# Optimization experiments

Measured on AMD Instinct MI355X. Metric: run time of the kernel, lower is better.

Reference implementation:

```python
import jax, jax.numpy as jnp
import numpy as np

B, T, D = 2, 2048, 1024
H, HD = 16, 64
DL, DC = 512, 256
THETA = 10000.0
LN_EPS = 1e-5


def setup_inputs() -> dict:
    key = jax.random.key(0)
    ks = jax.random.split(key, 8)
    s = 0.02
    return {
        "x": jax.random.normal(ks[0], (B, T, D), jnp.float32),
        "W_q": jax.random.normal(ks[1], (H * HD, D), jnp.float32) * s,
        "b_q": jnp.zeros((H * HD,), jnp.float32),
        "W_kvl": jax.random.normal(ks[2], (DL, D), jnp.float32) * s,
        "b_kvl": jnp.zeros((DL,), jnp.float32),
        "ts_scale": jnp.ones((DL,), jnp.float32),
        "ts_shift": jnp.zeros((DL,), jnp.float32),
        "W_comp": jax.random.normal(ks[3], (DC, DL), jnp.float32) * s,
        "W_exp": jax.random.normal(ks[4], (DL, DC), jnp.float32) * s,
        "ln_g": jnp.ones((DC,), jnp.float32),
        "ln_b": jnp.zeros((DC,), jnp.float32),
        "W_fkv": jax.random.normal(ks[5], (2 * H * HD, DL), jnp.float32) * s,
        "b_fkv": jnp.zeros((2 * H * HD,), jnp.float32),
        "W_out": jax.random.normal(ks[6], (D, H * HD), jnp.float32) * s,
        "b_out": jnp.zeros((D,), jnp.float32),
    }


def _rope_tables(t_len):
    inv_freq = 1.0 / (THETA ** (jnp.arange(0, HD, 2, dtype=jnp.float32) / HD))
    pos = jnp.arange(t_len, dtype=jnp.float32)
    freqs = pos[:, None] * inv_freq[None, :]          # [T, HD/2]
    cos = jnp.concatenate([jnp.cos(freqs)] * 2, -1)   # [T, HD]
    sin = jnp.concatenate([jnp.sin(freqs)] * 2, -1)
    return cos[None, None], sin[None, None]           # [1,1,T,HD]


def _rotate_half(z):
    return jnp.concatenate([-z[..., HD // 2:], z[..., :HD // 2]], -1)


def reference(x, W_q, b_q, W_kvl, b_kvl, ts_scale, ts_shift, W_comp, W_exp,
              ln_g, ln_b, W_fkv, b_fkv, W_out, b_out):
    # Q path: [B,T,D] -> [B,H,T,HD]
    q = (jnp.einsum('btd,ed->bte', x, W_q) + b_q).reshape(B, T, H, HD).transpose(0, 2, 1, 3)

    # KV latent + learned KVSplice bottleneck
    kvl = jnp.einsum('btd,ld->btl', x, W_kvl) + b_kvl                 # [B,T,DL]
    xt = kvl * jax.nn.softplus(ts_scale) + ts_shift
    c = jnp.einsum('btl,cl->btc', xt, W_comp)                         # [B,T,DC]
    mu = jnp.mean(c, -1, keepdims=True)
    var = jnp.mean(jnp.square(c - mu), -1, keepdims=True)
    c = (c - mu) * jax.lax.rsqrt(var + LN_EPS) * ln_g + ln_b
    dec = jnp.einsum('btc,lc->btl', c, W_exp)                         # [B,T,DL]

    # Decompress latent to K,V
    kv = jnp.einsum('btl,el->bte', dec, W_fkv) + b_fkv                # [B,T,2*H*HD]
    kv = kv.reshape(B, T, 2, H, HD).transpose(2, 0, 3, 1, 4)          # [2,B,H,T,HD]
    k, v = kv[0], kv[1]

    # RoPE
    cos, sin = _rope_tables(T)
    q = q * cos + _rotate_half(q) * sin
    k = k * cos + _rotate_half(k) * sin

    # Causal SDPA
    scale = 1.0 / np.sqrt(HD)
    scores = jnp.einsum('bhqd,bhkd->bhqk', q, k) * scale
    mask = jnp.tril(jnp.ones((T, T), bool))
    scores = jnp.where(mask, scores, jnp.float32(-1e30))
    attn = jax.nn.softmax(scores, axis=-1)
    o = jnp.einsum('bhqk,bhkd->bhqd', attn, v)
    o = o.transpose(0, 2, 1, 3).reshape(B, T, H * HD)
    return jnp.einsum('bte,de->btd', o, W_out) + b_out
```

## Files before the change

### kernel.cpp

```cpp
#include <hip/hip_runtime.h>
#include <math.h>

#define B_SZ   2
#define T_SEQ  2048
#define NH     16
#define HDIM   64
#define D_MOD  1024
#define DL     512
#define DC     256
#define MROWS  4096

typedef __attribute__((ext_vector_type(8))) short bf16x8;
typedef __attribute__((ext_vector_type(4))) float f32x4;

#define SCALE_Q 0.18033688011112042f

static __device__ __forceinline__ unsigned short f2bf(float f) {
    union { float f; unsigned u; } v; v.f = f;
    unsigned r = v.u + 0x7fffu + ((v.u >> 16) & 1u);
    return (unsigned short)(r >> 16);
}

static __device__ __forceinline__ void gl_lds16(const unsigned short* g,
                                                unsigned short* l) {
    __builtin_amdgcn_global_load_lds(
        (const __attribute__((address_space(1))) unsigned int*)g,
        (__attribute__((address_space(3))) unsigned int*)l, 16, 0, 0);
}

__global__ __launch_bounds__(256) void cvt_bf16(
    const float* __restrict__ x,  const float* __restrict__ wq,
    const float* __restrict__ wkvl, const float* __restrict__ wcomp,
    const float* __restrict__ wexp, const float* __restrict__ wfkv,
    const float* __restrict__ wout,
    unsigned short* __restrict__ xb,  unsigned short* __restrict__ wqh,
    unsigned short* __restrict__ wkvlh, unsigned short* __restrict__ wcomph,
    unsigned short* __restrict__ wexph, unsigned short* __restrict__ wfkvh,
    unsigned short* __restrict__ wouth, float2* __restrict__ rope_tab)
{
    const int g = blockIdx.x * 256 + threadIdx.x;
    const int stride = gridDim.x * 256;
#define CVT_SEG(src, dst, n4)                                              \
    for (int i = g; i < (n4); i += stride) {                               \
        float4 v = ((const float4*)(src))[i];                              \
        unsigned short h[4] = {f2bf(v.x), f2bf(v.y), f2bf(v.z), f2bf(v.w)};\
        *(uint2*)((dst) + (size_t)i * 4) = *(uint2*)h;                     \
    }
    CVT_SEG(x, xb, 1048576)
    CVT_SEG(wq, wqh, 262144)
    CVT_SEG(wkvl, wkvlh, 131072)
    CVT_SEG(wcomp, wcomph, 32768)
    CVT_SEG(wexp, wexph, 32768)
    CVT_SEG(wfkv, wfkvh, 262144)
    CVT_SEG(wout, wouth, 262144)
#undef CVT_SEG
    for (int i = g; i < T_SEQ * 32; i += stride) {
        const int t = i >> 5, fi = i & 31;
        const float inv = __expf((float)fi * (-9.210340371976184f / 32.0f));
        float sn, cs; sincosf((float)t * inv, &sn, &cs);
        rope_tab[i] = make_float2(cs, sn);
    }
}

#define GEMM64P_PROLOG(Aptr, Wptr, Kdim)                                       \
    __shared__ unsigned short As[2][64 * 64];                                  \
    __shared__ unsigned short Ws[2][64 * 64];                                  \
    const int tid = threadIdx.x;                                               \
    const int w = tid >> 6, lane = tid & 63;                                   \
    const int l16 = lane & 15, quad = lane >> 4;                               \
    const int sw8 = ((lane & 7) ^ ((lane >> 3) & 7)) << 3;                     \
    const int srow = lane >> 3;                                                \
    const unsigned short* Ag0 = (Aptr) + (size_t)(m0 + w * 16 + srow) * (Kdim) + sw8;      \
    const unsigned short* Ag1 = Ag0 + (size_t)8 * (Kdim);                      \
    const unsigned short* Wg0 = (Wptr) + (size_t)(n0 + w * 16 + srow) * (Kdim) + sw8;      \
    const unsigned short* Wg1 = Wg0 + (size_t)8 * (Kdim);                      \
    const int aoff = (w * 16) * 64;                                            \
    const int xh = (l16 & 7);                                                  \
    f32x4 acc[4];                                                              \
    _Pragma("unroll") for (int j = 0; j < 4; ++j)                              \
        acc[j] = (f32x4){0.f, 0.f, 0.f, 0.f};                                  \
    gl_lds16(Ag0, &As[0][aoff]);                                               \
    gl_lds16(Ag1, &As[0][aoff + 512]);                                         \
    gl_lds16(Wg0, &Ws[0][aoff]);                                               \
    gl_lds16(Wg1, &Ws[0][aoff + 512]);                                         \
    for (int k0 = 0, buf = 0; k0 < (Kdim); k0 += 64, buf ^= 1) {               \
        if (k0 + 64 < (Kdim)) {                                                \
            gl_lds16(Ag0 + k0 + 64, &As[buf ^ 1][aoff]);                       \
            gl_lds16(Ag1 + k0 + 64, &As[buf ^ 1][aoff + 512]);                 \
            gl_lds16(Wg0 + k0 + 64, &Ws[buf ^ 1][aoff]);                       \
            gl_lds16(Wg1 + k0 + 64, &Ws[buf ^ 1][aoff + 512]);                 \
            asm volatile("s_waitcnt vmcnt(4)" ::: "memory");                   \
        } else {                                                               \
            asm volatile("s_waitcnt vmcnt(0)" ::: "memory");                   \
        }                                                                      \
        __builtin_amdgcn_s_barrier();                                          \
        bf16x8 af[2], bfr[4][2];                                               \
        _Pragma("unroll") for (int kk = 0; kk < 2; ++kk)                       \
            af[kk] = *(const bf16x8*)&As[buf][(w * 16 + l16) * 64 +            \
                                         (((kk * 4 + quad) ^ xh) << 3)];       \
        _Pragma("unroll") for (int j = 0; j < 4; ++j)                          \
            _Pragma("unroll") for (int kk = 0; kk < 2; ++kk)                   \
                bfr[j][kk] = *(const bf16x8*)&Ws[buf][(j * 16 + l16) * 64 +    \
                                             (((kk * 4 + quad) ^ xh) << 3)];   \
        _Pragma("unroll") for (int kk = 0; kk < 2; ++kk)                       \
            _Pragma("unroll") for (int j = 0; j < 4; ++j)                      \
                acc[j] = __builtin_amdgcn_mfma_f32_16x16x32_bf16(              \
                    af[kk], bfr[j][kk], acc[j], 0, 0, 0);                      \
        asm volatile("s_waitcnt lgkmcnt(0)" ::: "memory");                     \
        __builtin_amdgcn_s_barrier();                                          \
    }

#define GEMM128x64P_PROLOG(Aptr, Wptr, Kdim)                                   \
    __shared__ unsigned short As[2][128 * 64];                                 \
    __shared__ unsigned short Ws[2][64 * 64];                                  \
    const int tid = threadIdx.x;                                               \
    const int w = tid >> 6, lane = tid & 63;                                   \
    const int l16 = lane & 15, quad = lane >> 4;                               \
    const int srow = lane >> 3;                                                \
    const int sw8 = ((lane & 7) ^ srow) << 3;                                  \
    const unsigned short* Ag = (Aptr) + (size_t)(m0 + w * 32 + srow) * (Kdim) + sw8; \
    const unsigned short* Wg = (Wptr) + (size_t)(n0 + w * 16 + srow) * (Kdim) + sw8; \
    const int xh = (l16 & 7);                                                  \
    f32x4 acc[2][4];                                                           \
    _Pragma("unroll") for (int mi = 0; mi < 2; ++mi)                           \
        _Pragma("unroll") for (int j = 0; j < 4; ++j)                          \
            acc[mi][j] = (f32x4){0.f, 0.f, 0.f, 0.f};                          \
    _Pragma("unroll") for (int seg = 0; seg < 4; ++seg)                        \
        gl_lds16(Ag + (size_t)(seg * 8) * (Kdim), &As[0][(w * 32 + seg * 8) * 64]); \
    _Pragma("unroll") for (int seg = 0; seg < 2; ++seg)                        \
        gl_lds16(Wg + (size_t)(seg * 8) * (Kdim), &Ws[0][(w * 16 + seg * 8) * 64]); \
    for (int k0 = 0, buf = 0; k0 < (Kdim); k0 += 64, buf ^= 1) {               \
        if (k0 + 64 < (Kdim)) {                                                \
            _Pragma("unroll") for (int seg = 0; seg < 4; ++seg)                \
                gl_lds16(Ag + (size_t)(seg * 8) * (Kdim) + k0 + 64,            \
                         &As[buf ^ 1][(w * 32 + seg * 8) * 64]);               \
            _Pragma("unroll") for (int seg = 0; seg < 2; ++seg)                \
                gl_lds16(Wg + (size_t)(seg * 8) * (Kdim) + k0 + 64,            \
                         &Ws[buf ^ 1][(w * 16 + seg * 8) * 64]);               \
            asm volatile("s_waitcnt vmcnt(6)" ::: "memory");                   \
        } else {                                                               \
            asm volatile("s_waitcnt vmcnt(0)" ::: "memory");                   \
        }                                                                      \
        __builtin_amdgcn_s_barrier();                                          \
        bf16x8 af[2][2], bfr[4][2];                                            \
        _Pragma("unroll") for (int mi = 0; mi < 2; ++mi)                       \
            _Pragma("unroll") for (int kk = 0; kk < 2; ++kk)                   \
                af[mi][kk] = *(const bf16x8*)&As[buf][(w * 32 + mi * 16 + l16) * 64 + \
                                             (((kk * 4 + quad) ^ xh) << 3)];   \
        _Pragma("unroll") for (int j = 0; j < 4; ++j)                          \
            _Pragma("unroll") for (int kk = 0; kk < 2; ++kk)                   \
                bfr[j][kk] = *(const bf16x8*)&Ws[buf][(j * 16 + l16) * 64 +    \
                                             (((kk * 4 + quad) ^ xh) << 3)];   \
        _Pragma("unroll") for (int kk = 0; kk < 2; ++kk)                       \
            _Pragma("unroll") for (int mi = 0; mi < 2; ++mi)                   \
                _Pragma("unroll") for (int j = 0; j < 4; ++j)                  \
                    acc[mi][j] = __builtin_amdgcn_mfma_f32_16x16x32_bf16(      \
                        af[mi][kk], bfr[j][kk], acc[mi][j], 0, 0, 0);          \
        asm volatile("s_waitcnt lgkmcnt(0)" ::: "memory");                     \
        __builtin_amdgcn_s_barrier();                                          \
    }

__global__ __launch_bounds__(256, 3) void gemm_qxt(
    const unsigned short* __restrict__ A, const unsigned short* __restrict__ Wq,
    const unsigned short* __restrict__ Wkvl,
    const float* __restrict__ b_q, const float* __restrict__ b_kvl,
    const float* __restrict__ ts_scale, const float* __restrict__ ts_shift,
    const float2* __restrict__ tab,
    unsigned short* __restrict__ qh, unsigned short* __restrict__ xt)
{
    const int m0 = blockIdx.x * 128;
    const bool is_q = (blockIdx.y < 16);
    const int n0 = is_q ? blockIdx.y * 64 : (blockIdx.y - 16) * 64;
    const unsigned short* W = is_q ? Wq : Wkvl;

    GEMM128x64P_PROLOG(A, W, D_MOD)

    if (is_q) {
#pragma unroll
        for (int j = 0; j < 4; ++j) {
            const int col = n0 + j * 16 + l16;
            const int h = col >> 6, hd = col & 63;
            const float bv = b_q[col];
            const float bvp = b_q[col ^ 32];
            const float sgn = (hd < 32) ? -1.f : 1.f;
#pragma unroll
            for (int mi = 0; mi < 2; ++mi) {
#pragma unroll
                for (int reg = 0; reg < 4; ++reg) {
                    const int row = m0 + w * 32 + mi * 16 + quad * 4 + reg;
                    const int b = row >> 11, t = row & (T_SEQ - 1);
                    const float2 cssn = tab[t * 32 + (hd & 31)];
                    const float v  = acc[mi][j][reg] + bv;
                    const float vp = acc[mi][j ^ 2][reg] + bvp;
                    const float r = (v * cssn.x + sgn * vp * cssn.y) * SCALE_Q;
                    qh[(((size_t)b * NH + h) * T_SEQ + t) * HDIM + hd] = f2bf(r);
                }
            }
        }
    } else {
#pragma unroll
        for (int j = 0; j < 4; ++j) {
            const int col = n0 + j * 16 + l16;
            const float bv = b_kvl[col];
            const float sp_s = log1pf(expf(ts_scale[col]));
            const float sp_t = ts_shift[col];
#pragma unroll
            for (int mi = 0; mi < 2; ++mi) {
#pragma unroll
                for (int reg = 0; reg < 4; ++reg) {
                    const int row = m0 + w * 32 + mi * 16 + quad * 4 + reg;
                    const float val = (acc[mi][j][reg] + bv) * sp_s + sp_t;
                    xt[(size_t)row * DL + col] = f2bf(val);
                }
            }
        }
    }
}

__global__ __launch_bounds__(256, 3) void gemm_kv(
    const unsigned short* __restrict__ A, const unsigned short* __restrict__ W,
    const float* __restrict__ bias, const float2* __restrict__ tab,
    unsigned short* __restrict__ kh, unsigned short* __restrict__ vth)
{
    const int m0 = blockIdx.x * 128, n0 = blockIdx.y * 64;

    GEMM128x64P_PROLOG(A, W, DL)

    if (n0 < 1024) {
#pragma unroll
        for (int j = 0; j < 4; ++j) {
            const int col = n0 + j * 16 + l16;
            const int h = (col >> 6) & 15, hd = col & 63;
            const float bv = bias[col];
            const float bvp = bias[col ^ 32];
            const float sgn = (hd < 32) ? -1.f : 1.f;
#pragma unroll
            for (int mi = 0; mi < 2; ++mi) {
#pragma unroll
                for (int reg = 0; reg < 4; ++reg) {
                    const int row = m0 + w * 32 + mi * 16 + quad * 4 + reg;
                    const int b = row >> 11, t = row & (T_SEQ - 1);
                    const float2 cssn = tab[t * 32 + (hd & 31)];
                    const float v  = acc[mi][j][reg] + bv;
                    const float vp = acc[mi][j ^ 2][reg] + bvp;
                    const float r = v * cssn.x + sgn * vp * cssn.y;
                    kh[(((size_t)b * NH + h) * T_SEQ + t) * HDIM + hd] = f2bf(r);
                }
            }
        }
    } else {
#pragma unroll
        for (int j = 0; j < 4; ++j) {
            const int col = n0 + j * 16 + l16;
            const int cv = col - 1024;
            const int h = cv >> 6, hd = cv & 63;
            const float bv = bias[col];
#pragma unroll
            for (int mi = 0; mi < 2; ++mi) {
                unsigned short hv[4];
                const int r0 = m0 + w * 32 + mi * 16 + quad * 4;
                const int b = r0 >> 11, t0 = r0 & (T_SEQ - 1);
#pragma unroll
                for (int reg = 0; reg < 4; ++reg)
                    hv[reg] = f2bf(acc[mi][j][reg] + bv);
                *(uint2*)&vth[(((size_t)b * NH + h) * HDIM + hd) * T_SEQ + t0] =
                    *(uint2*)hv;
            }
        }
    }
}

__global__ __launch_bounds__(256, 3) void gemm_out(
    const unsigned short* __restrict__ A, const unsigned short* __restrict__ W,
    const float* __restrict__ bias, float* __restrict__ C)
{
    const int m0 = blockIdx.x * 128, n0 = blockIdx.y * 64;

    GEMM128x64P_PROLOG(A, W, D_MOD)

#pragma unroll
    for (int j = 0; j < 4; ++j) {
        const int col = n0 + j * 16 + l16;
        const float bv = bias[col];
#pragma unroll
        for (int mi = 0; mi < 2; ++mi) {
#pragma unroll
            for (int reg = 0; reg < 4; ++reg) {
                const int row = m0 + w * 32 + mi * 16 + quad * 4 + reg;
                C[(size_t)row * D_MOD + col] = acc[mi][j][reg] + bv;
            }
        }
    }
}

__global__ __launch_bounds__(256) void gemm_b(
    const unsigned short* __restrict__ A, const unsigned short* __restrict__ W,
    unsigned short* __restrict__ dec)
{
    const int m0 = blockIdx.x * 64, n0 = blockIdx.y * 64;

    GEMM64P_PROLOG(A, W, DC)

#pragma unroll
    for (int j = 0; j < 4; ++j) {
        const int col = n0 + j * 16 + l16;
#pragma unroll
        for (int reg = 0; reg < 4; ++reg) {
            const int row = m0 + w * 16 + quad * 4 + reg;
            dec[(size_t)row * DL + col] = f2bf(acc[j][reg]);
        }
    }
}

__global__ __launch_bounds__(256) void gemm_c_ln(
    const unsigned short* __restrict__ A, const unsigned short* __restrict__ W,
    const float* __restrict__ g, const float* __restrict__ bta,
    unsigned short* __restrict__ outb)
{
    __shared__ unsigned short As[2][16 * 32];
    __shared__ unsigned short Ws[2][256 * 32];
    __shared__ float redS[4][16];
    __shared__ float redQ[4][16];

    const int tid = threadIdx.x;
    const int w = tid >> 6, lane = tid & 63;
    const int l16 = lane & 15, quad = lane >> 4;
    const int m0 = blockIdx.x * 16;

    const int srow = lane >> 2, scol = (lane & 3) << 3;
    const unsigned short* Ag = A + (size_t)(m0 + srow) * DL + scol;
    const unsigned short* Wg = W + (size_t)(w * 64 + srow) * DL + scol;

    f32x4 acc[4];
#pragma unroll
    for (int j = 0; j < 4; ++j) acc[j] = (f32x4){0.f, 0.f, 0.f, 0.f};

    if (w == 0) gl_lds16(Ag, &As[0][0]);
#pragma unroll
    for (int c = 0; c < 4; ++c)
        gl_lds16(Wg + (size_t)(c * 16) * DL, &Ws[0][(w * 64 + c * 16) * 32]);

    for (int k0 = 0, buf = 0; k0 < DL; k0 += 32, buf ^= 1) {
        if (k0 + 32 < DL) {
            if (w == 0) gl_lds16(Ag + k0 + 32, &As[buf ^ 1][0]);
#pragma unroll
            for (int c = 0; c < 4; ++c)
                gl_lds16(Wg + (size_t)(c * 16) * DL + k0 + 32,
                         &Ws[buf ^ 1][(w * 64 + c * 16) * 32]);
            if (w == 0) {
                asm volatile("s_waitcnt vmcnt(5)" ::: "memory");
            } else {
                asm volatile("s_waitcnt vmcnt(4)" ::: "memory");
            }
        } else {
            asm volatile("s_waitcnt vmcnt(0)" ::: "memory");
        }
        __builtin_amdgcn_s_barrier();

        const bf16x8 af = *(const bf16x8*)&As[buf][l16 * 32 + quad * 8];
        bf16x8 bfr[4];
#pragma unroll
        for (int j = 0; j < 4; ++j)
            bfr[j] = *(const bf16x8*)&Ws[buf][(w * 64 + j * 16 + l16) * 32 + quad * 8];
#pragma unroll
        for (int j = 0; j < 4; ++j)
            acc[j] = __builtin_amdgcn_mfma_f32_16x16x32_bf16(af, bfr[j], acc[j], 0, 0, 0);

        asm volatile("s_waitcnt lgkmcnt(0)" ::: "memory");
        __builtin_amdgcn_s_barrier();
    }

    float s[4], q2[4];
#pragma unroll
    for (int reg = 0; reg < 4; ++reg) {
        float sv = (acc[0][reg] + acc[1][reg]) + (acc[2][reg] + acc[3][reg]);
        float qv = (acc[0][reg] * acc[0][reg] + acc[1][reg] * acc[1][reg]) +
                   (acc[2][reg] * acc[2][reg] + acc[3][reg] * acc[3][reg]);
#pragma unroll
        for (int off = 1; off < 16; off <<= 1) {
            sv += __shfl_xor(sv, off);
            qv += __shfl_xor(qv, off);
        }
        s[reg] = sv; q2[reg] = qv;
    }
    if (l16 == 0) {
#pragma unroll
        for (int reg = 0; reg < 4; ++reg) {
            redS[w][quad * 4 + reg] = s[reg];
            redQ[w][quad * 4 + reg] = q2[reg];
        }
    }
    __syncthreads();

#pragma unroll
    for (int reg = 0; reg < 4; ++reg) {
        const int r = quad * 4 + reg;
        const float sum = (redS[0][r] + redS[1][r]) + (redS[2][r] + redS[3][r]);
        const float sq  = (redQ[0][r] + redQ[1][r]) + (redQ[2][r] + redQ[3][r]);
        const float mu  = sum * (1.0f / DC);
        const float var = sq * (1.0f / DC) - mu * mu;
        const float rstd = rsqrtf(var + 1e-5f);
#pragma unroll
        for (int j = 0; j < 4; ++j) {
            const int col = w * 64 + j * 16 + l16;
            const float val = (acc[j][reg] - mu) * rstd * g[col] + bta[col];
            outb[(size_t)(m0 + r) * DC + col] = f2bf(val);
        }
    }
}

__global__ __launch_bounds__(256, 4) void flash_mfma(
    const unsigned short* __restrict__ q, const unsigned short* __restrict__ k,
    const unsigned short* __restrict__ vt, unsigned short* __restrict__ o)
{
    __shared__ unsigned short Ks[2][64 * 64];
    __shared__ unsigned short Vs[2][64 * 64];
    __shared__ unsigned short Ps[64 * 64];

    const int bh = blockIdx.x & 31;
    const int j  = 31 - (blockIdx.x >> 5);
    const int q0 = j * 64;
    const int tid = threadIdx.x;
    const int w = tid >> 6, lane = tid & 63;
    const int l16 = lane & 15, quad = lane >> 4;
    const int rbase = q0 + w * 16;
    const int xh = l16 & 7;

    bf16x8 qf[2];
#pragma unroll
    for (int kk = 0; kk < 2; ++kk)
        qf[kk] = *(const bf16x8*)(q + ((size_t)bh * T_SEQ + rbase + l16) * HDIM + kk * 32 + quad * 8);

    f32x4 of[4];
    float lrow[4];
#pragma unroll
    for (int dt = 0; dt < 4; ++dt) of[dt] = (f32x4){0.f, 0.f, 0.f, 0.f};
#pragma unroll
    for (int r = 0; r < 4; ++r) lrow[r] = 0.f;

    const int ldr = tid >> 2;
    const int ldc = (tid & 3) * 16;
    const int sg0 = (((ldc >> 3) + 0) ^ (ldr & 7)) << 3;
    const int sg1 = (((ldc >> 3) + 1) ^ (ldr & 7)) << 3;
    const unsigned short* kgb = k + ((size_t)bh * T_SEQ + ldr) * HDIM + ldc;
    const unsigned short* vgb = vt + ((size_t)bh * HDIM + ldr) * T_SEQ + ldc;

    bf16x8 kr0 = *(const bf16x8*)kgb;
    bf16x8 kr1 = *(const bf16x8*)(kgb + 8);
    bf16x8 vr0 = *(const bf16x8*)vgb;
    bf16x8 vr1 = *(const bf16x8*)(vgb + 8);

    const int kend = (j + 1) * 64;
    int buf = 0;
    for (int k0 = 0; k0 < kend; k0 += 64, buf ^= 1) {
        *(bf16x8*)&Ks[buf][ldr * 64 + sg0] = kr0;
        *(bf16x8*)&Ks[buf][ldr * 64 + sg1] = kr1;
        *(bf16x8*)&Vs[buf][ldr * 64 + sg0] = vr0;
        *(bf16x8*)&Vs[buf][ldr * 64 + sg1] = vr1;
        if (k0 + 64 < kend) {
            const unsigned short* kg = kgb + (size_t)(k0 + 64) * HDIM;
            const unsigned short* vg = vgb + (k0 + 64);
            kr0 = *(const bf16x8*)kg;
            kr1 = *(const bf16x8*)(kg + 8);
            vr0 = *(const bf16x8*)vg;
            vr1 = *(const bf16x8*)(vg + 8);
        }
        __syncthreads();

        bf16x8 kf[4][2];
#pragma unroll
        for (int nt = 0; nt < 4; ++nt)
#pragma unroll
            for (int kk = 0; kk < 2; ++kk)
                kf[nt][kk] = *(const bf16x8*)&Ks[buf][(nt * 16 + l16) * 64 +
                                                     (((kk * 4 + quad) ^ xh) << 3)];

        f32x4 sf[4];
        __builtin_amdgcn_s_setprio(1);
#pragma unroll
        for (int nt = 0; nt < 4; ++nt) {
            sf[nt] = (f32x4){0.f, 0.f, 0.f, 0.f};
#pragma unroll
            for (int kk = 0; kk < 2; ++kk)
                sf[nt] = __builtin_amdgcn_mfma_f32_16x16x32_bf16(qf[kk], kf[nt][kk], sf[nt], 0, 0, 0);
        }
        __builtin_amdgcn_s_setprio(0);

        const bool need_mask = (k0 + 63) > rbase;
#pragma unroll
        for (int reg = 0; reg < 4; ++reg) {
            float a0 = sf[0][reg], a1 = sf[1][reg], a2 = sf[2][reg], a3 = sf[3][reg];
            if (need_mask) {
                const int tq = rbase + quad * 4 + reg;
                if (k0 +      l16 > tq) a0 = -1e30f;
                if (k0 + 16 + l16 > tq) a1 = -1e30f;
                if (k0 + 32 + l16 > tq) a2 = -1e30f;
                if (k0 + 48 + l16 > tq) a3 = -1e30f;
            }
            union { float f; unsigned u; } u0, u1, u2, u3;
            u0.f = exp2f(a0); u1.f = exp2f(a1);
            u2.f = exp2f(a2); u3.f = exp2f(a3);
            const int prow = w * 16 + quad * 4 + reg;
            const int pr7 = prow & 7;
            const int pb = prow * 64 + (l16 & 7);
            const int g0 = l16 >> 3;
            Ps[pb + (((0 + g0) ^ pr7) << 3)] = (unsigned short)(u0.u >> 16);
            Ps[pb + (((2 + g0) ^ pr7) << 3)] = (unsigned short)(u1.u >> 16);
            Ps[pb + (((4 + g0) ^ pr7) << 3)] = (unsigned short)(u2.u >> 16);
            Ps[pb + (((6 + g0) ^ pr7) << 3)] = (unsigned short)(u3.u >> 16);
            u0.u &= 0xffff0000u; u1.u &= 0xffff0000u;
            u2.u &= 0xffff0000u; u3.u &= 0xffff0000u;
            lrow[reg] += (u0.f + u1.f) + (u2.f + u3.f);
        }

        bf16x8 vf[4][2];
#pragma unroll
        for (int dt = 0; dt < 4; ++dt)
#pragma unroll
            for (int kk = 0; kk < 2; ++kk)
                vf[dt][kk] = *(const bf16x8*)&Vs[buf][(dt * 16 + l16) * 64 +
                                                     (((kk * 4 + quad) ^ xh) << 3)];

        bf16x8 pf[2];
#pragma unroll
        for (int kk = 0; kk < 2; ++kk)
            pf[kk] = *(const bf16x8*)&Ps[(w * 16 + l16) * 64 +
                                         (((kk * 4 + quad) ^ xh) << 3)];
        __builtin_amdgcn_s_setprio(1);
#pragma unroll
        for (int dt = 0; dt < 4; ++dt)
#pragma unroll
            for (int kk = 0; kk < 2; ++kk)
                of[dt] = __builtin_amdgcn_mfma_f32_16x16x32_bf16(pf[kk], vf[dt][kk], of[dt], 0, 0, 0);
        __builtin_amdgcn_s_setprio(0);
    }

    const int b = bh >> 4, h = bh & 15;
#pragma unroll
    for (int reg = 0; reg < 4; ++reg) {
        float l = lrow[reg];
        l += __shfl_xor(l, 1);
        l += __shfl_xor(l, 2);
        l += __shfl_xor(l, 4);
        l += __shfl_xor(l, 8);
        const float inv = 1.0f / l;
        const int t = rbase + quad * 4 + reg;
#pragma unroll
        for (int dt = 0; dt < 4; ++dt)
            o[((size_t)b * T_SEQ + t) * (NH * HDIM) + h * HDIM + dt * 16 + l16] =
                f2bf(of[dt][reg] * inv);
    }
}

extern "C" void kernel_launch(void* const* d_in, const int* in_sizes, int n_in,
                              void* d_out, int out_size, void* d_ws, size_t ws_size,
                              hipStream_t stream)
{
    (void)in_sizes; (void)n_in; (void)out_size; (void)ws_size;

    const float* x        = (const float*)d_in[0];
    const float* W_q      = (const float*)d_in[1];
    const float* b_q      = (const float*)d_in[2];
    const float* W_kvl    = (const float*)d_in[3];
    const float* b_kvl    = (const float*)d_in[4];
    const float* ts_scale = (const float*)d_in[5];
    const float* ts_shift = (const float*)d_in[6];
    const float* W_comp   = (const float*)d_in[7];
    const float* W_exp    = (const float*)d_in[8];
    const float* ln_g     = (const float*)d_in[9];
    const float* ln_b     = (const float*)d_in[10];
    const float* W_fkv    = (const float*)d_in[11];
    const float* b_fkv    = (const float*)d_in[12];
    const float* W_out    = (const float*)d_in[13];
    const float* b_out    = (const float*)d_in[14];
    float* out = (float*)d_out;

    char* p = (char*)d_ws;
    unsigned short* xb     = (unsigned short*)p;             p += 8  * 1024 * 1024;
    unsigned short* wqh    = (unsigned short*)p;             p += 2  * 1024 * 1024;
    unsigned short* wkvlh  = (unsigned short*)p;             p += 1  * 1024 * 1024;
    unsigned short* wcomph = (unsigned short*)p;             p += 256 * 1024;
    unsigned short* wexph  = (unsigned short*)p;             p += 256 * 1024;
    unsigned short* wfkvh  = (unsigned short*)p;             p += 2  * 1024 * 1024;
    unsigned short* wouth  = (unsigned short*)p;             p += 2  * 1024 * 1024;
    unsigned short* qh     = (unsigned short*)p;             p += 8  * 1024 * 1024;
    unsigned short* kh     = (unsigned short*)p;             p += 8  * 1024 * 1024;
    unsigned short* vth    = (unsigned short*)p;             p += 8  * 1024 * 1024;
    unsigned short* xt     = (unsigned short*)p;             p += 4  * 1024 * 1024;
    unsigned short* cbh    = (unsigned short*)p;             p += 2  * 1024 * 1024;
    unsigned short* dec    = (unsigned short*)p;             p += 4  * 1024 * 1024;
    unsigned short* ob     = (unsigned short*)p;             p += 8  * 1024 * 1024;
    float2*         tab    = (float2*)p;                     p += 512 * 1024;

    const dim3 blk(256);

    cvt_bf16<<<1024, blk, 0, stream>>>(x, W_q, W_kvl, W_comp, W_exp, W_fkv, W_out,
                                       xb, wqh, wkvlh, wcomph, wexph, wfkvh, wouth,
                                       tab);

    gemm_qxt<<<dim3(32, 24), blk, 0, stream>>>(
        xb, wqh, wkvlh, b_q, b_kvl, ts_scale, ts_shift, tab, qh, xt);

    gemm_c_ln<<<256, blk, 0, stream>>>(
        xt, wcomph, ln_g, ln_b, cbh);

    gemm_b<<<dim3(64, 8), blk, 0, stream>>>(
        cbh, wexph, dec);

    gemm_kv<<<dim3(32, 32), blk, 0, stream>>>(
        dec, wfkvh, b_fkv, tab, kh, vth);

    flash_mfma<<<1024, blk, 0, stream>>>(qh, kh, vth, ob);

    gemm_out<<<dim3(32, 16), blk, 0, stream>>>(
        ob, wouth, b_out, out);
}
```

Before: 209.8 us.

## Fold W_exp into W_fkv to skip the decompression GEMM

Precomputes a combined weight W_fkv·W_exp (2048x256) in a small GEMM over a transposed bf16 copy of W_exp, then runs the K/V projection directly on the 256-wide LayerNorm output. This removes the gemm_b kernel, the dec intermediate round-trip, and halves the K dimension of gemm_kv. In exchange a weight-only GEMM runs on every call, and rounding the combined weight to bf16 changes numerics slightly.

```diff
diff --git a/kernel.cpp b/kernel.cpp
--- a/kernel.cpp
+++ b/kernel.cpp
@@ -35,7 +35,7 @@
     const float* __restrict__ wout,
     unsigned short* __restrict__ xb,  unsigned short* __restrict__ wqh,
     unsigned short* __restrict__ wkvlh, unsigned short* __restrict__ wcomph,
-    unsigned short* __restrict__ wexph, unsigned short* __restrict__ wfkvh,
+    unsigned short* __restrict__ wexpTh, unsigned short* __restrict__ wfkvh,
     unsigned short* __restrict__ wouth, float2* __restrict__ rope_tab)
 {
     const int g = blockIdx.x * 256 + threadIdx.x;
@@ -50,10 +50,17 @@
     CVT_SEG(wq, wqh, 262144)
     CVT_SEG(wkvl, wkvlh, 131072)
     CVT_SEG(wcomp, wcomph, 32768)
-    CVT_SEG(wexp, wexph, 32768)
     CVT_SEG(wfkv, wfkvh, 262144)
     CVT_SEG(wout, wouth, 262144)
 #undef CVT_SEG
+    for (int i = g; i < 32768; i += stride) {
+        const int c = i >> 7, l4 = (i & 127) << 2;
+        unsigned short h[4];
+#pragma unroll
+        for (int r = 0; r < 4; ++r)
+            h[r] = f2bf(wexp[(size_t)(l4 + r) * DC + c]);
+        *(uint2*)(wexpTh + (size_t)c * DL + l4) = *(uint2*)h;
+    }
     for (int i = g; i < T_SEQ * 32; i += stride) {
         const int t = i >> 5, fi = i & 31;
         const float inv = __expf((float)fi * (-9.210340371976184f / 32.0f));
@@ -217,6 +224,26 @@
     }
 }
 
+__global__ __launch_bounds__(256) void gemm_wcomb(
+    const unsigned short* __restrict__ A,
+    const unsigned short* __restrict__ W,
+    unsigned short* __restrict__ wcomb)
+{
+    const int m0 = blockIdx.x * 64, n0 = blockIdx.y * 64;
+
+    GEMM64P_PROLOG(A, W, DL)
+
+#pragma unroll
+    for (int j = 0; j < 4; ++j) {
+        const int col = n0 + j * 16 + l16;
+#pragma unroll
+        for (int reg = 0; reg < 4; ++reg) {
+            const int row = m0 + w * 16 + quad * 4 + reg;
+            wcomb[(size_t)row * DC + col] = f2bf(acc[j][reg]);
+        }
+    }
+}
+
 __global__ __launch_bounds__(256, 3) void gemm_kv(
     const unsigned short* __restrict__ A, const unsigned short* __restrict__ W,
     const float* __restrict__ bias, const float2* __restrict__ tab,
@@ -224,7 +251,7 @@
 {
     const int m0 = blockIdx.x * 128, n0 = blockIdx.y * 64;
 
-    GEMM128x64P_PROLOG(A, W, DL)
+    GEMM128x64P_PROLOG(A, W, DC)
 
     if (n0 < 1024) {
 #pragma unroll
@@ -289,25 +316,6 @@
                 const int row = m0 + w * 32 + mi * 16 + quad * 4 + reg;
                 C[(size_t)row * D_MOD + col] = acc[mi][j][reg] + bv;
             }
-        }
-    }
-}
-
-__global__ __launch_bounds__(256) void gemm_b(
-    const unsigned short* __restrict__ A, const unsigned short* __restrict__ W,
-    unsigned short* __restrict__ dec)
-{
-    const int m0 = blockIdx.x * 64, n0 = blockIdx.y * 64;
-
-    GEMM64P_PROLOG(A, W, DC)
-
-#pragma unroll
-    for (int j = 0; j < 4; ++j) {
-        const int col = n0 + j * 16 + l16;
-#pragma unroll
-        for (int reg = 0; reg < 4; ++reg) {
-            const int row = m0 + w * 16 + quad * 4 + reg;
-            dec[(size_t)row * DL + col] = f2bf(acc[j][reg]);
         }
     }
 }
@@ -580,7 +588,7 @@
     unsigned short* wqh    = (unsigned short*)p;             p += 2  * 1024 * 1024;
     unsigned short* wkvlh  = (unsigned short*)p;             p += 1  * 1024 * 1024;
     unsigned short* wcomph = (unsigned short*)p;             p += 256 * 1024;
-    unsigned short* wexph  = (unsigned short*)p;             p += 256 * 1024;
+    unsigned short* wexpTh = (unsigned short*)p;             p += 256 * 1024;
     unsigned short* wfkvh  = (unsigned short*)p;             p += 2  * 1024 * 1024;
     unsigned short* wouth  = (unsigned short*)p;             p += 2  * 1024 * 1024;
     unsigned short* qh     = (unsigned short*)p;             p += 8  * 1024 * 1024;
@@ -588,15 +596,18 @@
     unsigned short* vth    = (unsigned short*)p;             p += 8  * 1024 * 1024;
     unsigned short* xt     = (unsigned short*)p;             p += 4  * 1024 * 1024;
     unsigned short* cbh    = (unsigned short*)p;             p += 2  * 1024 * 1024;
-    unsigned short* dec    = (unsigned short*)p;             p += 4  * 1024 * 1024;
+    unsigned short* wcombh = (unsigned short*)p;             p += 4  * 1024 * 1024;
     unsigned short* ob     = (unsigned short*)p;             p += 8  * 1024 * 1024;
     float2*         tab    = (float2*)p;                     p += 512 * 1024;
 
     const dim3 blk(256);
 
     cvt_bf16<<<1024, blk, 0, stream>>>(x, W_q, W_kvl, W_comp, W_exp, W_fkv, W_out,
-                                       xb, wqh, wkvlh, wcomph, wexph, wfkvh, wouth,
+                                       xb, wqh, wkvlh, wcomph, wexpTh, wfkvh, wouth,
                                        tab);
+
+    gemm_wcomb<<<dim3(32, 4), blk, 0, stream>>>(
+        wfkvh, wexpTh, wcombh);
 
     gemm_qxt<<<dim3(32, 24), blk, 0, stream>>>(
         xb, wqh, wkvlh, b_q, b_kvl, ts_scale, ts_shift, tab, qh, xt);
@@ -604,11 +615,8 @@
     gemm_c_ln<<<256, blk, 0, stream>>>(
         xt, wcomph, ln_g, ln_b, cbh);
 
-    gemm_b<<<dim3(64, 8), blk, 0, stream>>>(
-        cbh, wexph, dec);
-
     gemm_kv<<<dim3(32, 32), blk, 0, stream>>>(
-        dec, wfkvh, b_fkv, tab, kh, vth);
+        cbh, wcombh, b_fkv, tab, kh, vth);
 
     flash_mfma<<<1024, blk, 0, stream>>>(qh, kh, vth, ob);
 
```

Result: no change. 209.4 us (-0.2%).
